# Kernel optimization log

Measured on AMD Instinct MI355X. Metric: run time of the kernel, lower is better.

## Reference

```python
import jax, jax.numpy as jnp
import numpy as np

DIM = 768
HEADS = 12
HIDDEN = 4 * DIM
EPS = 1e-5


def _layernorm(x, g, b):
    mu = jnp.mean(x, axis=-1, keepdims=True)
    var = jnp.var(x, axis=-1, keepdims=True)
    return (x - mu) * jax.lax.rsqrt(var + EPS) * g + b


def setup_inputs() -> dict:
    key = jax.random.key(0)
    ks = jax.random.split(key, 8)
    B, N, C = 16, 577, DIM
    s = lambda fan: 1.0 / np.sqrt(fan)
    return {
        "x": jax.random.normal(ks[0], (B, N, C), jnp.float32),
        "ln1_g": jnp.ones((C,), jnp.float32),
        "ln1_b": jnp.zeros((C,), jnp.float32),
        "qkv_w": jax.random.normal(ks[1], (C, 3 * C), jnp.float32) * s(C),
        "qkv_b": jnp.zeros((3 * C,), jnp.float32),
        "proj_w": jax.random.normal(ks[2], (C, C), jnp.float32) * s(C),
        "proj_b": jnp.zeros((C,), jnp.float32),
        "ln2_g": jnp.ones((C,), jnp.float32),
        "ln2_b": jnp.zeros((C,), jnp.float32),
        "fc1_w": jax.random.normal(ks[3], (C, HIDDEN), jnp.float32) * s(C),
        "fc1_b": jnp.zeros((HIDDEN,), jnp.float32),
        "fc2_w": jax.random.normal(ks[4], (HIDDEN, C), jnp.float32) * s(HIDDEN),
        "fc2_b": jnp.zeros((C,), jnp.float32),
    }


def reference(x, ln1_g, ln1_b, qkv_w, qkv_b, proj_w, proj_b,
              ln2_g, ln2_b, fc1_w, fc1_b, fc2_w, fc2_b):
    B, N, C = x.shape
    H = HEADS
    Dh = C // H
    scale = Dh ** (-0.5)

    # --- attention branch (pre-norm) ---
    xn = _layernorm(x, ln1_g, ln1_b)
    qkv = xn @ qkv_w + qkv_b                         # [B,N,3C]
    qkv = qkv.reshape(B, N, 3, H, Dh).transpose(2, 0, 3, 1, 4)  # [3,B,H,N,Dh]
    q, k, v = qkv[0], qkv[1], qkv[2]
    attn = jax.nn.softmax(jnp.einsum('bhnd,bhmd->bhnm', q, k) * scale, axis=-1)
    y = jnp.einsum('bhnm,bhmd->bhnd', attn, v)       # [B,H,N,Dh]
    y = y.transpose(0, 2, 1, 3).reshape(B, N, C)
    y = y @ proj_w + proj_b
    x = x + y

    # --- MLP branch (pre-norm, exact GELU as torch default) ---
    xn2 = _layernorm(x, ln2_g, ln2_b)
    h = jax.nn.gelu(xn2 @ fc1_w + fc1_b, approximate=False)
    x = x + (h @ fc2_w + fc2_b)
    return x
```

## Files before the change

kernel.cpp:

```cpp
#include <hip/hip_runtime.h>
#include <hip/hip_bf16.h>
#include <math.h>


#define C_DIM   768
#define SEQ     577
#define BATCH   16
#define NHEAD   12
#define DHEAD   64
#define MREAL   (BATCH*SEQ)
#define MPAD    9344
#define HID     3072
#define QKW     1536
#define NKV     640
#define QSCALE  0.1803368801111204f

typedef __hip_bfloat16 bf16;
typedef __attribute__((ext_vector_type(8))) short v8s;
typedef __attribute__((ext_vector_type(4))) float v4f;

static __device__ __forceinline__ bf16 f2b(float f){ return __float2bfloat16(f); }
static __device__ __forceinline__ float us2f(unsigned short u){
  union{ float f; unsigned int i; } x; x.i = ((unsigned int)u)<<16; return x.f;
}
static __device__ __forceinline__ short f2s(float f){
  bf16 t = __float2bfloat16(f); return *(short*)&t;
}


__global__ __launch_bounds__(256) void k_transpose_cast(
    const float* __restrict__ src, bf16* __restrict__ dst, int R, int C)
{
  __shared__ float s[64][65];
  const int tr = blockIdx.x*64, tc = blockIdx.y*64;
  const int t = threadIdx.x;
  const int lr = t >> 4, lc4 = t & 15;
  #pragma unroll
  for (int i=0;i<4;i++){
    int r = lr + i*16;
    float4 v = *(const float4*)(src + (size_t)(tr+r)*C + tc + lc4*4);
    s[r][lc4*4+0]=v.x; s[r][lc4*4+1]=v.y; s[r][lc4*4+2]=v.z; s[r][lc4*4+3]=v.w;
  }
  __syncthreads();
  const int c = t >> 2, seg = t & 3;
  alignas(16) bf16 tmp[16];
  #pragma unroll
  for (int j=0;j<16;j++) tmp[j] = f2b(s[seg*16+j][c]);
  bf16* dp = dst + (size_t)(tc+c)*R + tr + seg*16;
  *(uint4*)dp       = *(uint4*)tmp;
  *(uint4*)(dp + 8) = *(uint4*)(tmp + 8);
}

__global__ __launch_bounds__(256) void k_zero_pad(bf16* __restrict__ y)
{
  size_t i = (size_t)blockIdx.x*256 + threadIdx.x;
  y[(size_t)MREAL*C_DIM + i] = f2b(0.f);
}

__global__ __launch_bounds__(256) void k_layernorm(
    const float* __restrict__ in, const float* __restrict__ g,
    const float* __restrict__ b, bf16* __restrict__ o)
{
  int row = blockIdx.x, tid = threadIdx.x;
  size_t base = (size_t)row*C_DIM;
  if (row >= MREAL){
    #pragma unroll
    for (int j=0;j<3;j++) o[base + tid + j*256] = f2b(0.f);
    return;
  }
  float v[3], s=0.f, ss=0.f;
  #pragma unroll
  for (int j=0;j<3;j++){ v[j] = in[base + tid + j*256]; s += v[j]; ss += v[j]*v[j]; }
  #pragma unroll
  for (int off=32; off>0; off>>=1){ s += __shfl_xor(s,off); ss += __shfl_xor(ss,off); }
  __shared__ float red[8];
  int wv = tid>>6;
  if ((tid&63)==0){ red[wv] = s; red[4+wv] = ss; }
  __syncthreads();
  float S  = red[0]+red[1]+red[2]+red[3];
  float SS = red[4]+red[5]+red[6]+red[7];
  float mu   = S*(1.f/C_DIM);
  float rstd = rsqrtf(SS*(1.f/C_DIM) - mu*mu + 1e-5f);
  #pragma unroll
  for (int j=0;j<3;j++){
    int c = tid + j*256;
    o[base+c] = f2b((v[j]-mu)*rstd*g[c] + b[c]);
  }
}

__global__ __launch_bounds__(256, 3) void k_flash(
    const bf16* __restrict__ qk, const bf16* __restrict__ VtAll,
    bf16* __restrict__ y)
{
  __shared__ alignas(16) bf16 sK[2][64*64];
  __shared__ alignas(16) bf16 sV[2][64*64];
  __shared__ alignas(16) bf16 sP[4][16*72];

  const int tid = threadIdx.x;
  const int wave = tid>>6, lane = tid&63;
  const int r16 = lane&15, kg = lane>>4;

  const int id = blockIdx.x;
  const int swz = (id&7)*240 + (id>>3);
  const int hh = swz/10, qt = swz - hh*10;
  const int b_ = hh/NHEAD, h_ = hh - b_*NHEAD;

  const int qrow = b_*SEQ + qt*64 + wave*16 + r16;
  v8s qf[2];
  qf[0] = *(const v8s*)(qk + (size_t)qrow*QKW + h_*DHEAD + kg*8);
  qf[1] = *(const v8s*)(qk + (size_t)qrow*QKW + h_*DHEAD + 32 + kg*8);

  auto stage = [&](int kt, int buf){
    #pragma unroll
    for (int i=0;i<2;i++){
      int chunk = i*256 + tid;
      int row = chunk>>3, ch = chunk&7;
      int sc = ch ^ (row&7);
      const bf16* gk = qk + (size_t)(b_*SEQ + kt*64 + row)*QKW
                          + C_DIM + h_*DHEAD + sc*8;
      const bf16* gv = VtAll + (size_t)(b_*C_DIM + h_*DHEAD + row)*NKV
                             + kt*64 + sc*8;
      __builtin_amdgcn_global_load_lds(
          (const __attribute__((address_space(1))) void*)gk,
          (__attribute__((address_space(3))) void*)((char*)&sK[buf][0] + i*4096 + wave*1024),
          16, 0, 0);
      __builtin_amdgcn_global_load_lds(
          (const __attribute__((address_space(1))) void*)gv,
          (__attribute__((address_space(3))) void*)((char*)&sV[buf][0] + i*4096 + wave*1024),
          16, 0, 0);
    }
  };

  float m_run = -1e30f, l_run = 0.f;
  v4f zero4 = {0.f,0.f,0.f,0.f};
  v4f o[4] = {zero4, zero4, zero4, zero4};

  stage(0, 0);
  for (int kt=0; kt<10; ++kt){
    __syncthreads();
    if (kt < 9) stage(kt+1, (kt+1)&1);
    const bf16* Kt = &sK[kt&1][0];
    const bf16* Vt = &sV[kt&1][0];

    v4f sfr[4] = {zero4, zero4, zero4, zero4};
    #pragma unroll
    for (int ks=0; ks<2; ++ks){
      #pragma unroll
      for (int m=0;m<4;m++){
        int key = m*16 + r16;
        v8s kf = *(const v8s*)(Kt + key*64 + (((ks*4+kg) ^ (key&7))*8));
        sfr[m] = __builtin_amdgcn_mfma_f32_16x16x32_bf16(kf, qf[ks], sfr[m], 0, 0, 0);
      }
    }

    if (kt == 9){
      #pragma unroll
      for (int m=0;m<4;m++)
        #pragma unroll
        for (int gg=0; gg<4; ++gg){
          int kb = 576 + m*16 + kg*4 + gg;
          if (kb >= SEQ) sfr[m][gg] = -1e30f;
        }
    }

    float tmax = -1e30f;
    #pragma unroll
    for (int m=0;m<4;m++)
      #pragma unroll
      for (int gg=0; gg<4; ++gg) tmax = fmaxf(tmax, sfr[m][gg]);
    tmax = fmaxf(tmax, __shfl_xor(tmax, 16));
    tmax = fmaxf(tmax, __shfl_xor(tmax, 32));
    float mn  = fmaxf(m_run, tmax);
    float scl = exp2f(m_run - mn);
    float ps  = 0.f;
    #pragma unroll
    for (int m=0;m<4;m++)
      #pragma unroll
      for (int gg=0; gg<4; ++gg){
        float pv = exp2f(sfr[m][gg] - mn);
        sfr[m][gg] = pv; ps += pv;
      }
    ps += __shfl_xor(ps, 16);
    ps += __shfl_xor(ps, 32);
    l_run = l_run*scl + ps;
    m_run = mn;
    #pragma unroll
    for (int mf=0; mf<4; ++mf) o[mf] *= scl;

    bf16* Pw = &sP[wave][0];
    #pragma unroll
    for (int m=0;m<4;m++){
      short4 w;
      w.x = f2s(sfr[m][0]); w.y = f2s(sfr[m][1]);
      w.z = f2s(sfr[m][2]); w.w = f2s(sfr[m][3]);
      *(short4*)(Pw + r16*72 + m*16 + kg*4) = w;
    }
    asm volatile("s_waitcnt lgkmcnt(0)" ::: "memory");
    v8s pb0 = *(const v8s*)(Pw + r16*72 + kg*8);
    v8s pb1 = *(const v8s*)(Pw + r16*72 + 32 + kg*8);
    #pragma unroll
    for (int mf=0; mf<4; ++mf){
      int d = mf*16 + r16;
      v8s v0 = *(const v8s*)(Vt + d*64 + ((kg     ^ (d&7))*8));
      v8s v1 = *(const v8s*)(Vt + d*64 + (((4+kg) ^ (d&7))*8));
      o[mf] = __builtin_amdgcn_mfma_f32_16x16x32_bf16(v0, pb0, o[mf], 0, 0, 0);
      o[mf] = __builtin_amdgcn_mfma_f32_16x16x32_bf16(v1, pb1, o[mf], 0, 0, 0);
    }
  }

  const int qg = qt*64 + wave*16 + r16;
  if (qg < SEQ){
    float inv = 1.f / l_run;
    #pragma unroll
    for (int mf=0; mf<4; ++mf){
      short4 w;
      w.x = f2s(o[mf][0]*inv); w.y = f2s(o[mf][1]*inv);
      w.z = f2s(o[mf][2]*inv); w.w = f2s(o[mf][3]*inv);
      *(short4*)(y + (size_t)(b_*SEQ + qg)*C_DIM + h_*DHEAD + mf*16 + kg*4) = w;
    }
  }
}

template<int EPI>
__global__ __launch_bounds__(256, 4) void gemm_bt(
    const bf16* __restrict__ A, int lda,
    const bf16* __restrict__ BT, int ldb,
    void* Cv, int ldc,
    const float* __restrict__ bias,
    const float* resid,
    int K)
{
  __shared__ alignas(16) bf16 sA[128*64];
  __shared__ alignas(16) bf16 sB[128*64];
  const int tid  = threadIdx.x;
  const int wave = tid>>6, lane = tid&63;
  const int wr = wave>>1, wc = wave&1;
  const int r16 = lane&15, kg = lane>>4;

  int nx = gridDim.x, nwg = nx*gridDim.y;
  int id = blockIdx.y*nx + blockIdx.x;
  int qq = nwg>>3, r8 = nwg&7, xcd = id&7, j = id>>3;
  int swz = (xcd<r8 ? xcd*(qq+1) : r8*(qq+1) + (xcd-r8)*qq) + j;
  int mt = swz / nx, nt = swz % nx;

  v4f acc[4][4];
  v4f zero4 = {0.f,0.f,0.f,0.f};
  #pragma unroll
  for (int m=0;m<4;m++)
    #pragma unroll
    for (int n=0;n<4;n++) acc[m][n] = zero4;

  const int mrow0 = mt*128, ncol0 = nt*128;

  for (int kt=0; kt<K; kt+=64){
    #pragma unroll
    for (int i=0;i<4;i++){
      int ci = wave*4 + i;
      int q  = ci*64 + lane;
      int rr = q>>3;
      int cc = (q&7)*8;
      const bf16* ga = A  + (size_t)(mrow0+rr)*lda + (kt+cc);
      const bf16* gb = BT + (size_t)(ncol0+rr)*ldb + (kt+cc);
      __builtin_amdgcn_global_load_lds(
          (const __attribute__((address_space(1))) void*)ga,
          (__attribute__((address_space(3))) void*)((char*)sA + ci*1024), 16, 0, 0);
      __builtin_amdgcn_global_load_lds(
          (const __attribute__((address_space(1))) void*)gb,
          (__attribute__((address_space(3))) void*)((char*)sB + ci*1024), 16, 0, 0);
    }
    __syncthreads();
    #pragma unroll
    for (int ks=0; ks<2; ks++){
      v8s av[4], bv[4];
      #pragma unroll
      for (int m=0;m<4;m++)
        av[m] = *(const v8s*)(sA + (wr*64 + m*16 + r16)*64 + ks*32 + kg*8);
      #pragma unroll
      for (int n=0;n<4;n++)
        bv[n] = *(const v8s*)(sB + (wc*64 + n*16 + r16)*64 + ks*32 + kg*8);
      #pragma unroll
      for (int m=0;m<4;m++)
        #pragma unroll
        for (int n=0;n<4;n++)
          acc[m][n] = __builtin_amdgcn_mfma_f32_16x16x32_bf16(av[m], bv[n], acc[m][n], 0, 0, 0);
    }
    __syncthreads();
  }

  #pragma unroll
  for (int m=0;m<4;m++){
    #pragma unroll
    for (int n=0;n<4;n++){
      int col = ncol0 + wc*64 + n*16 + r16;
      #pragma unroll
      for (int gg=0; gg<4; gg++){
        int row = mrow0 + wr*64 + m*16 + kg*4 + gg;
        float v = acc[m][n][gg];
        if constexpr (EPI==0){
          float oo = v + bias[col];
          if (col < C_DIM) oo *= QSCALE;
          ((bf16*)Cv)[(size_t)row*ldc + col] = f2b(oo);
        } else if constexpr (EPI==1){
          float xg = v + bias[col];
          float oo = 0.5f*xg*(1.f + erff(xg*0.70710678118654752f));
          ((bf16*)Cv)[(size_t)row*ldc + col] = f2b(oo);
        } else if constexpr (EPI==2){
          if (row < MREAL){
            size_t idx = (size_t)row*ldc + col;
            ((float*)Cv)[idx] = v + bias[col] + resid[idx];
          }
        } else {
          int g = col;
          if (g < MREAL){
            int b = g / SEQ;
            int key = g - b*SEQ;
            ((bf16*)Cv)[((size_t)b*C_DIM + row)*NKV + key] = f2b(v + bias[row]);
          }
        }
      }
    }
  }
}


extern "C" void kernel_launch(void* const* d_in, const int* in_sizes, int n_in,
                              void* d_out, int out_size, void* d_ws, size_t ws_size,
                              hipStream_t stream)
{
  const float* x     = (const float*)d_in[0];
  const float* ln1g  = (const float*)d_in[1];
  const float* ln1b  = (const float*)d_in[2];
  const float* qkvw  = (const float*)d_in[3];
  const float* qkvb  = (const float*)d_in[4];
  const float* projw = (const float*)d_in[5];
  const float* projb = (const float*)d_in[6];
  const float* ln2g  = (const float*)d_in[7];
  const float* ln2b  = (const float*)d_in[8];
  const float* fc1w  = (const float*)d_in[9];
  const float* fc1b  = (const float*)d_in[10];
  const float* fc2w  = (const float*)d_in[11];
  const float* fc2b  = (const float*)d_in[12];
  float* out = (float*)d_out;

  char* p = (char*)d_ws;
  auto take = [&](size_t n){ char* r = p; p += (n + 255) & ~(size_t)255; return r; };
  bf16* qkvT = (bf16*)take((size_t)(3*C_DIM)*C_DIM*2);
  bf16* projT= (bf16*)take((size_t)C_DIM*C_DIM*2);
  bf16* fc1T = (bf16*)take((size_t)HID*C_DIM*2);
  bf16* fc2T = (bf16*)take((size_t)C_DIM*HID*2);
  bf16* xn   = (bf16*)take((size_t)MPAD*C_DIM*2);
  bf16* xn2  = (bf16*)take((size_t)MPAD*C_DIM*2);
  bf16* qk   = (bf16*)take((size_t)MPAD*QKW*2);
  bf16* y    = (bf16*)take((size_t)MPAD*C_DIM*2);
  bf16* h    = (bf16*)take((size_t)MPAD*HID*2);
  bf16* VtAll= (bf16*)take((size_t)(BATCH*C_DIM + 2*DHEAD)*NKV*2);

  k_transpose_cast<<<dim3(C_DIM/64, 3*C_DIM/64), 256, 0, stream>>>(qkvw, qkvT, C_DIM, 3*C_DIM);
  k_transpose_cast<<<dim3(C_DIM/64, C_DIM/64),  256, 0, stream>>>(projw, projT, C_DIM, C_DIM);
  k_transpose_cast<<<dim3(C_DIM/64, HID/64),    256, 0, stream>>>(fc1w, fc1T, C_DIM, HID);
  k_transpose_cast<<<dim3(HID/64,  C_DIM/64),   256, 0, stream>>>(fc2w, fc2T, HID, C_DIM);
  k_zero_pad<<<336, 256, 0, stream>>>(y);

  k_layernorm<<<MPAD, 256, 0, stream>>>(x, ln1g, ln1b, xn);

  gemm_bt<0><<<dim3(QKW/128, MPAD/128), 256, 0, stream>>>(
      xn, C_DIM, qkvT, C_DIM, qk, QKW, qkvb, nullptr, C_DIM);

  gemm_bt<5><<<dim3(MPAD/128, C_DIM/128), 256, 0, stream>>>(
      qkvT + (size_t)QKW*C_DIM, C_DIM, xn, C_DIM, VtAll, 0,
      qkvb + 2*C_DIM, nullptr, C_DIM);

  k_flash<<<1920, 256, 0, stream>>>(qk, VtAll, y);

  gemm_bt<2><<<dim3(C_DIM/128, MPAD/128), 256, 0, stream>>>(
      y, C_DIM, projT, C_DIM, out, C_DIM, projb, x, C_DIM);

  k_layernorm<<<MPAD, 256, 0, stream>>>(out, ln2g, ln2b, xn2);

  gemm_bt<1><<<dim3(HID/128, MPAD/128), 256, 0, stream>>>(
      xn2, C_DIM, fc1T, C_DIM, h, HID, fc1b, nullptr, C_DIM);

  gemm_bt<2><<<dim3(C_DIM/128, MPAD/128), 256, 0, stream>>>(
      h, HID, fc2T, HID, out, C_DIM, fc2b, out, HID);
}
```

Before: 340.8 us.

## Replace GEMMs with 256x256 eight-wave pipelined kernel and split-K fc2

Replaces the 128x128 four-wave GEMM with a 256x256 tile kernel using eight waves. It streams K in 32-wide slices through a 4-deep LDS ring with XOR-swizzled columns, interleaves global-to-LDS staging with MFMA bursts, and raises MFMA priority with setprio. The row padding grows to a multiple of 256. The fc2 GEMM is split along K into two halves that write bf16 partials into the reused qk buffer, and a new reduction kernel adds the partials, bias and residual. The aim is more data reuse per tile and hidden load latency. In exchange, grids are much smaller (for example 111 blocks for proj), LDS use is large, and the split-K partials are rounded to bf16, which costs some precision.

Result: slower. 356.5 us (+4.6%).

```diff
diff --git a/kernel.cpp b/kernel.cpp
--- a/kernel.cpp
+++ b/kernel.cpp
@@ -9,7 +9,7 @@
 #define NHEAD   12
 #define DHEAD   64
 #define MREAL   (BATCH*SEQ)
-#define MPAD    9344
+#define MPAD    9472
 #define HID     3072
 #define QKW     1536
 #define NKV     640
@@ -86,6 +86,23 @@
     int c = tid + j*256;
     o[base+c] = f2b((v[j]-mu)*rstd*g[c] + b[c]);
   }
+}
+
+__global__ __launch_bounds__(256) void k_reduce2(
+    const bf16* __restrict__ P, const float* __restrict__ bias,
+    float* __restrict__ out)
+{
+  size_t i = ((size_t)blockIdx.x*256 + threadIdx.x)*8;
+  int c = (int)(i % C_DIM);
+  v8s p0 = *(const v8s*)(P + i);
+  v8s p1 = *(const v8s*)(P + (size_t)MPAD*C_DIM + i);
+  float r[8];
+  #pragma unroll
+  for (int j=0;j<8;j++) r[j] = out[i+j];
+  #pragma unroll
+  for (int j=0;j<8;j++)
+    out[i+j] = us2f((unsigned short)p0[j]) + us2f((unsigned short)p1[j])
+             + bias[c+j] + r[j];
 }
 
 __global__ __launch_bounds__(256, 3) void k_flash(
@@ -222,79 +239,126 @@
 }
 
 template<int EPI>
-__global__ __launch_bounds__(256, 4) void gemm_bt(
+__global__ __launch_bounds__(512, 2) void gemm8(
     const bf16* __restrict__ A, int lda,
     const bf16* __restrict__ BT, int ldb,
     void* Cv, int ldc,
     const float* __restrict__ bias,
-    const float* resid,
+    const float* __restrict__ resid,
     int K)
 {
-  __shared__ alignas(16) bf16 sA[128*64];
-  __shared__ alignas(16) bf16 sB[128*64];
-  const int tid  = threadIdx.x;
-  const int wave = tid>>6, lane = tid&63;
-  const int wr = wave>>1, wc = wave&1;
+  __shared__ bf16 sA[4][8192];
+  __shared__ bf16 sB[4][8192];
+  const int tid = threadIdx.x;
+  const int lane = tid&63, wave = tid>>6;
+  const int wm = wave>>2, wn = wave&3;
   const int r16 = lane&15, kg = lane>>4;
 
   int nx = gridDim.x, nwg = nx*gridDim.y;
   int id = blockIdx.y*nx + blockIdx.x;
-  int qq = nwg>>3, r8 = nwg&7, xcd = id&7, j = id>>3;
-  int swz = (xcd<r8 ? xcd*(qq+1) : r8*(qq+1) + (xcd-r8)*qq) + j;
+  int qq = nwg>>3, r8 = nwg&7, xcd = id&7, jj = id>>3;
+  int swz = (xcd<r8 ? xcd*(qq+1) : r8*(qq+1) + (xcd-r8)*qq) + jj;
   int mt = swz / nx, nt = swz % nx;
-
-  v4f acc[4][4];
+  const int mrow0 = mt*256, ncol0 = nt*256;
+
+  const bf16* Ap = A  + (size_t)mrow0*lda;
+  const bf16* Bp = BT + (size_t)ncol0*ldb;
+  int kbase = 0;
+  if constexpr (EPI==6) kbase = blockIdx.z * K;
+
+  const int srow  = tid>>2;
+  const int scol8 = ((tid&3) ^ ((srow>>1)&3))*8;
+
+#define STAGE_A(T2, H) {                                                      \
+    const bf16* g_ = Ap + (size_t)((H)*128 + srow)*lda + (kbase + (T2)*32 + scol8); \
+    __builtin_amdgcn_global_load_lds(                                          \
+        (const __attribute__((address_space(1))) void*)g_,                     \
+        (__attribute__((address_space(3))) void*)((char*)&sA[(T2)&3][0] + (H)*8192 + tid*16), \
+        16, 0, 0); }
+#define STAGE_B(T2, H) {                                                      \
+    const bf16* g_ = Bp + (size_t)((H)*128 + srow)*ldb + (kbase + (T2)*32 + scol8); \
+    __builtin_amdgcn_global_load_lds(                                          \
+        (const __attribute__((address_space(1))) void*)g_,                     \
+        (__attribute__((address_space(3))) void*)((char*)&sB[(T2)&3][0] + (H)*8192 + tid*16), \
+        16, 0, 0); }
+
+  v4f acc[8][4];
   v4f zero4 = {0.f,0.f,0.f,0.f};
   #pragma unroll
-  for (int m=0;m<4;m++)
+  for (int m=0;m<8;m++)
     #pragma unroll
     for (int n=0;n<4;n++) acc[m][n] = zero4;
 
-  const int mrow0 = mt*128, ncol0 = nt*128;
-
-  for (int kt=0; kt<K; kt+=64){
-    #pragma unroll
-    for (int i=0;i<4;i++){
-      int ci = wave*4 + i;
-      int q  = ci*64 + lane;
-      int rr = q>>3;
-      int cc = (q&7)*8;
-      const bf16* ga = A  + (size_t)(mrow0+rr)*lda + (kt+cc);
-      const bf16* gb = BT + (size_t)(ncol0+rr)*ldb + (kt+cc);
-      __builtin_amdgcn_global_load_lds(
-          (const __attribute__((address_space(1))) void*)ga,
-          (__attribute__((address_space(3))) void*)((char*)sA + ci*1024), 16, 0, 0);
-      __builtin_amdgcn_global_load_lds(
-          (const __attribute__((address_space(1))) void*)gb,
-          (__attribute__((address_space(3))) void*)((char*)sB + ci*1024), 16, 0, 0);
-    }
-    __syncthreads();
-    #pragma unroll
-    for (int ks=0; ks<2; ks++){
-      v8s av[4], bv[4];
+  const int NK = K >> 5;
+
+  STAGE_A(0,0) STAGE_A(0,1) STAGE_B(0,0) STAGE_B(0,1)
+  STAGE_A(1,0) STAGE_A(1,1) STAGE_B(1,0) STAGE_B(1,1)
+  STAGE_A(2,0) STAGE_A(2,1) STAGE_B(2,0) STAGE_B(2,1)
+  asm volatile("s_waitcnt vmcnt(8)" ::: "memory");
+  __builtin_amdgcn_s_barrier();
+
+#define G8_GROUP(T, DO_STAGE, WAITASM)                                        \
+  {                                                                           \
+    const int s_ = (T)&3;                                                     \
+    v8s aA[4], bB[4], aA2[4];                                                 \
+    _Pragma("unroll")                                                         \
+    for (int m=0;m<4;m++){                                                    \
+      int row = wm*128 + m*16 + r16;                                          \
+      aA[m] = *(const v8s*)(&sA[s_][row*32 + ((kg ^ ((row>>1)&3))<<3)]);      \
+    }                                                                         \
+    _Pragma("unroll")                                                         \
+    for (int n=0;n<4;n++){                                                    \
+      int row = wn*64 + n*16 + r16;                                           \
+      bB[n] = *(const v8s*)(&sB[s_][row*32 + ((kg ^ ((row>>1)&3))<<3)]);      \
+    }                                                                         \
+    if (DO_STAGE){ STAGE_A((T)+3, 0) STAGE_A((T)+3, 1) }                      \
+    __builtin_amdgcn_s_barrier();                                             \
+    asm volatile("s_waitcnt lgkmcnt(0)" ::: "memory");                        \
+    __builtin_amdgcn_s_setprio(1);                                            \
+    _Pragma("unroll")                                                         \
+    for (int m=0;m<4;m++)                                                     \
+      _Pragma("unroll")                                                       \
+      for (int n=0;n<4;n++)                                                   \
+        acc[m][n] = __builtin_amdgcn_mfma_f32_16x16x32_bf16(aA[m], bB[n], acc[m][n], 0,0,0); \
+    __builtin_amdgcn_s_setprio(0);                                            \
+    __builtin_amdgcn_s_barrier();                                             \
+    _Pragma("unroll")                                                         \
+    for (int m=0;m<4;m++){                                                    \
+      int row = wm*128 + (m+4)*16 + r16;                                      \
+      aA2[m] = *(const v8s*)(&sA[s_][row*32 + ((kg ^ ((row>>1)&3))<<3)]);     \
+    }                                                                         \
+    if (DO_STAGE){ STAGE_B((T)+3, 0) STAGE_B((T)+3, 1) }                      \
+    __builtin_amdgcn_s_barrier();                                             \
+    asm volatile("s_waitcnt lgkmcnt(0)" ::: "memory");                        \
+    __builtin_amdgcn_s_setprio(1);                                            \
+    _Pragma("unroll")                                                         \
+    for (int m=0;m<4;m++)                                                     \
+      _Pragma("unroll")                                                       \
+      for (int n=0;n<4;n++)                                                   \
+        acc[m+4][n] = __builtin_amdgcn_mfma_f32_16x16x32_bf16(aA2[m], bB[n], acc[m+4][n], 0,0,0); \
+    __builtin_amdgcn_s_setprio(0);                                            \
+    WAITASM;                                                                  \
+    __builtin_amdgcn_s_barrier();                                             \
+  }
+
+  for (int t=0; t<NK-3; ++t)
+    G8_GROUP(t, true, asm volatile("s_waitcnt vmcnt(8)" ::: "memory"))
+  G8_GROUP(NK-3, false, asm volatile("s_waitcnt vmcnt(4)" ::: "memory"))
+  G8_GROUP(NK-2, false, asm volatile("s_waitcnt vmcnt(0)" ::: "memory"))
+  G8_GROUP(NK-1, false, )
+
+#undef G8_GROUP
+#undef STAGE_A
+#undef STAGE_B
+
+  #pragma unroll
+  for (int m=0;m<8;m++){
+    #pragma unroll
+    for (int n=0;n<4;n++){
+      int col = ncol0 + wn*64 + n*16 + r16;
       #pragma unroll
-      for (int m=0;m<4;m++)
-        av[m] = *(const v8s*)(sA + (wr*64 + m*16 + r16)*64 + ks*32 + kg*8);
-      #pragma unroll
-      for (int n=0;n<4;n++)
-        bv[n] = *(const v8s*)(sB + (wc*64 + n*16 + r16)*64 + ks*32 + kg*8);
-      #pragma unroll
-      for (int m=0;m<4;m++)
-        #pragma unroll
-        for (int n=0;n<4;n++)
-          acc[m][n] = __builtin_amdgcn_mfma_f32_16x16x32_bf16(av[m], bv[n], acc[m][n], 0, 0, 0);
-    }
-    __syncthreads();
-  }
-
-  #pragma unroll
-  for (int m=0;m<4;m++){
-    #pragma unroll
-    for (int n=0;n<4;n++){
-      int col = ncol0 + wc*64 + n*16 + r16;
-      #pragma unroll
-      for (int gg=0; gg<4; gg++){
-        int row = mrow0 + wr*64 + m*16 + kg*4 + gg;
+      for (int gg=0; gg<4; ++gg){
+        int row = mrow0 + wm*128 + m*16 + kg*4 + gg;
         float v = acc[m][n][gg];
         if constexpr (EPI==0){
           float oo = v + bias[col];
@@ -309,13 +373,15 @@
             size_t idx = (size_t)row*ldc + col;
             ((float*)Cv)[idx] = v + bias[col] + resid[idx];
           }
-        } else {
+        } else if constexpr (EPI==5){
           int g = col;
           if (g < MREAL){
             int b = g / SEQ;
             int key = g - b*SEQ;
             ((bf16*)Cv)[((size_t)b*C_DIM + row)*NKV + key] = f2b(v + bias[row]);
           }
+        } else {
+          ((bf16*)Cv)[(size_t)blockIdx.z*MPAD*C_DIM + (size_t)row*ldc + col] = f2b(v);
         }
       }
     }
@@ -354,32 +420,34 @@
   bf16* y    = (bf16*)take((size_t)MPAD*C_DIM*2);
   bf16* h    = (bf16*)take((size_t)MPAD*HID*2);
   bf16* VtAll= (bf16*)take((size_t)(BATCH*C_DIM + 2*DHEAD)*NKV*2);
+  bf16* P    = qk;
 
   k_transpose_cast<<<dim3(C_DIM/64, 3*C_DIM/64), 256, 0, stream>>>(qkvw, qkvT, C_DIM, 3*C_DIM);
   k_transpose_cast<<<dim3(C_DIM/64, C_DIM/64),  256, 0, stream>>>(projw, projT, C_DIM, C_DIM);
   k_transpose_cast<<<dim3(C_DIM/64, HID/64),    256, 0, stream>>>(fc1w, fc1T, C_DIM, HID);
   k_transpose_cast<<<dim3(HID/64,  C_DIM/64),   256, 0, stream>>>(fc2w, fc2T, HID, C_DIM);
-  k_zero_pad<<<336, 256, 0, stream>>>(y);
+  k_zero_pad<<<(MPAD-MREAL)*C_DIM/256, 256, 0, stream>>>(y);
 
   k_layernorm<<<MPAD, 256, 0, stream>>>(x, ln1g, ln1b, xn);
 
-  gemm_bt<0><<<dim3(QKW/128, MPAD/128), 256, 0, stream>>>(
+  gemm8<0><<<dim3(QKW/256, MPAD/256), 512, 0, stream>>>(
       xn, C_DIM, qkvT, C_DIM, qk, QKW, qkvb, nullptr, C_DIM);
 
-  gemm_bt<5><<<dim3(MPAD/128, C_DIM/128), 256, 0, stream>>>(
+  gemm8<5><<<dim3(MPAD/256, C_DIM/256), 512, 0, stream>>>(
       qkvT + (size_t)QKW*C_DIM, C_DIM, xn, C_DIM, VtAll, 0,
       qkvb + 2*C_DIM, nullptr, C_DIM);
 
   k_flash<<<1920, 256, 0, stream>>>(qk, VtAll, y);
 
-  gemm_bt<2><<<dim3(C_DIM/128, MPAD/128), 256, 0, stream>>>(
+  gemm8<2><<<dim3(C_DIM/256, MPAD/256), 512, 0, stream>>>(
       y, C_DIM, projT, C_DIM, out, C_DIM, projb, x, C_DIM);
 
   k_layernorm<<<MPAD, 256, 0, stream>>>(out, ln2g, ln2b, xn2);
 
-  gemm_bt<1><<<dim3(HID/128, MPAD/128), 256, 0, stream>>>(
+  gemm8<1><<<dim3(HID/256, MPAD/256), 512, 0, stream>>>(
       xn2, C_DIM, fc1T, C_DIM, h, HID, fc1b, nullptr, C_DIM);
 
-  gemm_bt<2><<<dim3(C_DIM/128, MPAD/128), 256, 0, stream>>>(
-      h, HID, fc2T, HID, out, C_DIM, fc2b, out, HID);
-}
+  gemm8<6><<<dim3(C_DIM/256, MPAD/256, 2), 512, 0, stream>>>(
+      h, HID, fc2T, HID, P, C_DIM, nullptr, nullptr, HID/2);
+  k_reduce2<<<(MREAL*C_DIM)/(256*8), 256, 0, stream>>>(P, fc2b, out);
+}
```
